# Kernel tuning notes

Hardware: AMD Instinct MI355X
Metric: run time of the kernel (lower is better)

Reference implementation:

```python
import jax, jax.numpy as jnp
import numpy as np

OUTPUT_LEN = 128

def setup_inputs() -> dict:
    key = jax.random.key(0)
    k1, k2, k3 = jax.random.split(key, 3)
    B, D = 256, 1024
    scale = 1.0 / np.sqrt(D)
    x = jax.random.normal(k1, (B, D), dtype=jnp.float32)
    W = jax.random.normal(k2, (D, 3 * D), dtype=jnp.float32) * scale  # input kernel [d, 3d] (z|r|h)
    U = jax.random.normal(k3, (D, 3 * D), dtype=jnp.float32) * scale  # recurrent kernel [d, 3d]
    b = jnp.zeros((3 * D,), dtype=jnp.float32)
    return {"x": x, "W": W, "U": U, "b": b}

def _gru_cell(inp, h, W, U, b):
    # Classic GRU (reset_after=False), Keras gate order z, r, h and
    # update rule h_new = z * h + (1 - z) * hh.
    gx = inp @ W + b              # [B, 3d]
    gh = h @ U                    # [B, 3d]
    xz, xr, xh = jnp.split(gx, 3, axis=-1)
    hz, hr, hh_lin = jnp.split(gh, 3, axis=-1)
    z = jax.nn.sigmoid(xz + hz)
    r = jax.nn.sigmoid(xr + hr)
    hh = jnp.tanh(xh + r * hh_lin)
    return z * h + (1.0 - z) * hh

def reference(x, W, U, b):
    # x: [B, d] is the initial GRU state; the first step's input is zeros,
    # afterwards each step's output (== new state) is fed back as input.
    def step(carry, _):
        inp, h = carry
        new_h = _gru_cell(inp, h, W, U, b)
        return (new_h, new_h), new_h

    init = (jnp.zeros_like(x), x)
    _, outs = jax.lax.scan(step, init, None, length=OUTPUT_LEN)  # [T, B, d]
    return jnp.transpose(outs, (1, 0, 2))  # [B, T, d]
```

## Files before the change

kernel.cpp:

```cpp
#include <hip/hip_runtime.h>
#include <stdint.h>

#define B_ROWS 256
#define DDIM   1024
#define TSTEPS 128
#define THREE_D 3072

typedef short bf16x8 __attribute__((ext_vector_type(8)));
typedef float f32x4  __attribute__((ext_vector_type(4)));
typedef unsigned short u16x8 __attribute__((ext_vector_type(8)));

static __device__ __forceinline__ unsigned short f2bf(float f) {
    union { float f; uint32_t u; } v; v.f = f;
    uint32_t u = v.u;
    uint32_t r = u + 0x7FFFu + ((u >> 16) & 1u);
    return (unsigned short)(r >> 16);
}
static __device__ __forceinline__ float bf2f(unsigned short h) {
    union { uint32_t u; float f; } v; v.u = ((uint32_t)h) << 16; return v.f;
}

__global__ __launch_bounds__(256) void pack_kernel(
    const float* __restrict__ W, const float* __restrict__ U,
    unsigned short* __restrict__ phi, unsigned short* __restrict__ plo)
{
    int t = blockIdx.x * 256 + threadIdx.x;
    int lane  = t & 63;
    int ktile = (t >> 6) & 31;
    int ntile = t >> 11;
    int col = ntile * 16 + (lane & 15);
    int q = col >> 10;
    int d = col & 1023;
    int k8 = ktile * 32 + ((lane >> 4) << 3);

    u16x8 ohi, olo;
    #pragma unroll
    for (int j = 0; j < 8; ++j) {
        int k = k8 + j;
        const float* wr = W + (size_t)k * THREE_D;
        const float* ur = U + (size_t)k * THREE_D;
        float v;
        if (q == 0)      v = wr[d] + ur[d];
        else if (q == 1) v = wr[1024 + d] + ur[1024 + d];
        else if (q == 2) v = wr[2048 + d];
        else             v = ur[2048 + d];
        unsigned short hi = f2bf(v);
        ohi[j] = hi;
        olo[j] = f2bf(v - bf2f(hi));
    }
    size_t base = ((size_t)(ntile * 32 + ktile) * 64 + lane) * 8;
    *(u16x8*)(phi + base) = ohi;
    *(u16x8*)(plo + base) = olo;
}

__global__ __launch_bounds__(256) void gru_step0(
    const float* __restrict__ x, const float* __restrict__ U,
    const float* __restrict__ bias,
    float* __restrict__ out,
    unsigned short* __restrict__ hbh, unsigned short* __restrict__ hbl)
{
    __shared__ float xt[16][64];
    const int tid = threadIdx.x;
    const int c   = tid & 63;
    const int rg  = tid >> 6;
    const int dt  = blockIdx.x & 15;
    const int rt  = blockIdx.x >> 4;

    float acc[4][3];
    #pragma unroll
    for (int rr = 0; rr < 4; ++rr) { acc[rr][0] = 0.f; acc[rr][1] = 0.f; acc[rr][2] = 0.f; }

    for (int kc = 0; kc < 16; ++kc) {
        #pragma unroll
        for (int i = 0; i < 4; ++i) {
            int e = i * 256 + tid;
            int row = e >> 6, kk = e & 63;
            xt[row][kk] = x[(size_t)(rt * 16 + row) * DDIM + kc * 64 + kk];
        }
        __syncthreads();
        #pragma unroll 4
        for (int kk = 0; kk < 64; ++kk) {
            int k = kc * 64 + kk;
            const float* up = U + (size_t)k * THREE_D + dt * 64 + c;
            float uz = up[0], ur = up[1024], uh = up[2048];
            #pragma unroll
            for (int rr = 0; rr < 4; ++rr) {
                float xv = xt[rg * 4 + rr][kk];
                acc[rr][0] += xv * uz;
                acc[rr][1] += xv * ur;
                acc[rr][2] += xv * uh;
            }
        }
        __syncthreads();
    }

    int d = dt * 64 + c;
    #pragma unroll
    for (int rr = 0; rr < 4; ++rr) {
        int row = rt * 16 + rg * 4 + rr;
        float z  = 1.0f / (1.0f + __expf(-(acc[rr][0] + bias[d])));
        float r  = 1.0f / (1.0f + __expf(-(acc[rr][1] + bias[1024 + d])));
        float hh = tanhf(bias[2048 + d] + r * acc[rr][2]);
        float hp = x[(size_t)row * DDIM + d];
        float hn = z * hp + (1.0f - z) * hh;
        out[(size_t)row * (TSTEPS * DDIM) + d] = hn;
        unsigned short hi = f2bf(hn);
        size_t off = (size_t)row * DDIM + d;
        hbh[off] = hi;
        hbl[off] = f2bf(hn - bf2f(hi));
    }
}

__global__ __launch_bounds__(256) void gru_step(
    const unsigned short* __restrict__ phi,
    const unsigned short* __restrict__ plo,
    const unsigned short* __restrict__ hbh_in,
    const unsigned short* __restrict__ hbl_in,
    const float* __restrict__ bias,
    float* __restrict__ out,
    unsigned short* __restrict__ hbh_out,
    unsigned short* __restrict__ hbl_out,
    int t)
{
    __shared__ float gbuf[4][64][16];
    const int tid  = threadIdx.x;
    const int lane = tid & 63;
    const int q    = tid >> 6;
    const int dt   = blockIdx.x & 63;
    const int rt   = blockIdx.x >> 6;
    const int llow = lane & 15;
    const int lhi  = lane >> 4;

    f32x4 acc[4] = {f32x4{0,0,0,0}, f32x4{0,0,0,0}, f32x4{0,0,0,0}, f32x4{0,0,0,0}};

    const int ntile = q * 64 + dt;
    const unsigned short* bhp = phi + ((size_t)ntile * 2048 + lane) * 8;
    const unsigned short* blp = plo + ((size_t)ntile * 2048 + lane) * 8;
    const unsigned short* ahp = hbh_in + (size_t)(rt * 64 + llow) * DDIM + lhi * 8;
    const unsigned short* alp = hbl_in + (size_t)(rt * 64 + llow) * DDIM + lhi * 8;

    #pragma unroll 2
    for (int kt = 0; kt < 32; ++kt) {
        bf16x8 bh = *(const bf16x8*)(bhp + (size_t)kt * 512);
        bf16x8 bl = *(const bf16x8*)(blp + (size_t)kt * 512);
        const int koff = kt * 32;
        #pragma unroll
        for (int m = 0; m < 4; ++m) {
            bf16x8 ah = *(const bf16x8*)(ahp + (size_t)m * 16 * DDIM + koff);
            bf16x8 al = *(const bf16x8*)(alp + (size_t)m * 16 * DDIM + koff);
            acc[m] = __builtin_amdgcn_mfma_f32_16x16x32_bf16(ah, bh, acc[m], 0, 0, 0);
            acc[m] = __builtin_amdgcn_mfma_f32_16x16x32_bf16(al, bh, acc[m], 0, 0, 0);
            acc[m] = __builtin_amdgcn_mfma_f32_16x16x32_bf16(ah, bl, acc[m], 0, 0, 0);
        }
    }

    #pragma unroll
    for (int m = 0; m < 4; ++m) {
        #pragma unroll
        for (int r = 0; r < 4; ++r) {
            gbuf[q][m * 16 + lhi * 4 + r][llow] = acc[m][r];
        }
    }
    __syncthreads();

    #pragma unroll
    for (int i = 0; i < 4; ++i) {
        int e = tid + i * 256;
        int row = e >> 4, col = e & 15;
        int d = dt * 16 + col;
        int grow = rt * 64 + row;
        float gz = gbuf[0][row][col] + bias[d];
        float gr = gbuf[1][row][col] + bias[1024 + d];
        float gx = gbuf[2][row][col] + bias[2048 + d];
        float gu = gbuf[3][row][col];
        float z  = 1.0f / (1.0f + __expf(-gz));
        float r  = 1.0f / (1.0f + __expf(-gr));
        float hh = tanhf(gx + r * gu);
        size_t orow = (size_t)grow * (TSTEPS * DDIM);
        float hp = out[orow + (size_t)(t - 1) * DDIM + d];
        float hn = z * hp + (1.0f - z) * hh;
        out[orow + (size_t)t * DDIM + d] = hn;
        unsigned short hi = f2bf(hn);
        size_t hoff = (size_t)grow * DDIM + d;
        hbh_out[hoff] = hi;
        hbl_out[hoff] = f2bf(hn - bf2f(hi));
    }
}

extern "C" void kernel_launch(void* const* d_in, const int* in_sizes, int n_in,
                              void* d_out, int out_size, void* d_ws, size_t ws_size,
                              hipStream_t stream) {
    const float* x = (const float*)d_in[0];
    const float* W = (const float*)d_in[1];
    const float* U = (const float*)d_in[2];
    const float* b = (const float*)d_in[3];
    float* out = (float*)d_out;

    char* ws = (char*)d_ws;
    unsigned short* phi = (unsigned short*)ws;
    unsigned short* plo = (unsigned short*)(ws + (8u << 20));
    char* hbase = ws + (16u << 20);
    unsigned short* hbh[2] = { (unsigned short*)hbase,
                               (unsigned short*)(hbase + (512u << 10)) };
    unsigned short* hbl[2] = { (unsigned short*)(hbase + (1024u << 10)),
                               (unsigned short*)(hbase + (1536u << 10)) };

    hipLaunchKernelGGL(pack_kernel, dim3(2048), dim3(256), 0, stream, W, U, phi, plo);
    hipLaunchKernelGGL(gru_step0, dim3(256), dim3(256), 0, stream, x, U, b,
                       out, hbh[0], hbl[0]);

    for (int t = 1; t < TSTEPS; ++t) {
        int src = (t - 1) & 1;
        int dst = t & 1;
        hipLaunchKernelGGL(gru_step, dim3(256), dim3(256), 0, stream,
                           phi, plo, hbh[src], hbl[src], b,
                           out, hbh[dst], hbl[dst], t);
    }
}
```

Measured before the change: 4.673 ms.

## Fuse all GRU steps into one persistent cooperative kernel with resident weights

Replaces the pack kernel, step-0 kernel and 127 per-step launches with a single cooperative persistent kernel of 256 blocks. Each block keeps its slice of the packed weights on chip for all steps, the high bf16 half in LDS and the low half in registers, and keeps the previous state in registers. Steps are separated by per-row-group atomic counter barriers instead of kernel boundaries. This removes launch overhead and the repeated weight reads from global memory, at the cost of spin-wait barriers, high register and LDS pressure, and a reliance on all 256 blocks being co-resident.

```diff
diff --git a/kernel.cpp b/kernel.cpp
--- a/kernel.cpp
+++ b/kernel.cpp
@@ -1,14 +1,13 @@
 #include <hip/hip_runtime.h>
 #include <stdint.h>
 
-#define B_ROWS 256
-#define DDIM   1024
-#define TSTEPS 128
+
+#define DDIM    1024
 #define THREE_D 3072
+#define TSTEPS  128
 
 typedef short bf16x8 __attribute__((ext_vector_type(8)));
 typedef float f32x4  __attribute__((ext_vector_type(4)));
-typedef unsigned short u16x8 __attribute__((ext_vector_type(8)));
 
 static __device__ __forceinline__ unsigned short f2bf(float f) {
     union { float f; uint32_t u; } v; v.f = f;
@@ -19,110 +18,25 @@
 static __device__ __forceinline__ float bf2f(unsigned short h) {
     union { uint32_t u; float f; } v; v.u = ((uint32_t)h) << 16; return v.f;
 }
-
-__global__ __launch_bounds__(256) void pack_kernel(
-    const float* __restrict__ W, const float* __restrict__ U,
-    unsigned short* __restrict__ phi, unsigned short* __restrict__ plo)
-{
-    int t = blockIdx.x * 256 + threadIdx.x;
-    int lane  = t & 63;
-    int ktile = (t >> 6) & 31;
-    int ntile = t >> 11;
-    int col = ntile * 16 + (lane & 15);
-    int q = col >> 10;
-    int d = col & 1023;
-    int k8 = ktile * 32 + ((lane >> 4) << 3);
-
-    u16x8 ohi, olo;
+static __device__ __forceinline__ void split8(const float* v, bf16x8& hi, bf16x8& lo) {
     #pragma unroll
     for (int j = 0; j < 8; ++j) {
-        int k = k8 + j;
-        const float* wr = W + (size_t)k * THREE_D;
-        const float* ur = U + (size_t)k * THREE_D;
-        float v;
-        if (q == 0)      v = wr[d] + ur[d];
-        else if (q == 1) v = wr[1024 + d] + ur[1024 + d];
-        else if (q == 2) v = wr[2048 + d];
-        else             v = ur[2048 + d];
-        unsigned short hi = f2bf(v);
-        ohi[j] = hi;
-        olo[j] = f2bf(v - bf2f(hi));
-    }
-    size_t base = ((size_t)(ntile * 32 + ktile) * 64 + lane) * 8;
-    *(u16x8*)(phi + base) = ohi;
-    *(u16x8*)(plo + base) = olo;
-}
-
-__global__ __launch_bounds__(256) void gru_step0(
-    const float* __restrict__ x, const float* __restrict__ U,
-    const float* __restrict__ bias,
-    float* __restrict__ out,
-    unsigned short* __restrict__ hbh, unsigned short* __restrict__ hbl)
+        unsigned short h = f2bf(v[j]);
+        hi[j] = (short)h;
+        lo[j] = (short)f2bf(v[j] - bf2f(h));
+    }
+}
+
+__global__ __launch_bounds__(256, 1) void gru_persistent(
+    const float* __restrict__ x, const float* __restrict__ W,
+    const float* __restrict__ U, const float* __restrict__ bias,
+    float* __restrict__ out, unsigned short* __restrict__ hb,
+    int* __restrict__ syncc)
 {
-    __shared__ float xt[16][64];
-    const int tid = threadIdx.x;
-    const int c   = tid & 63;
-    const int rg  = tid >> 6;
-    const int dt  = blockIdx.x & 15;
-    const int rt  = blockIdx.x >> 4;
-
-    float acc[4][3];
-    #pragma unroll
-    for (int rr = 0; rr < 4; ++rr) { acc[rr][0] = 0.f; acc[rr][1] = 0.f; acc[rr][2] = 0.f; }
-
-    for (int kc = 0; kc < 16; ++kc) {
-        #pragma unroll
-        for (int i = 0; i < 4; ++i) {
-            int e = i * 256 + tid;
-            int row = e >> 6, kk = e & 63;
-            xt[row][kk] = x[(size_t)(rt * 16 + row) * DDIM + kc * 64 + kk];
-        }
-        __syncthreads();
-        #pragma unroll 4
-        for (int kk = 0; kk < 64; ++kk) {
-            int k = kc * 64 + kk;
-            const float* up = U + (size_t)k * THREE_D + dt * 64 + c;
-            float uz = up[0], ur = up[1024], uh = up[2048];
-            #pragma unroll
-            for (int rr = 0; rr < 4; ++rr) {
-                float xv = xt[rg * 4 + rr][kk];
-                acc[rr][0] += xv * uz;
-                acc[rr][1] += xv * ur;
-                acc[rr][2] += xv * uh;
-            }
-        }
-        __syncthreads();
-    }
-
-    int d = dt * 64 + c;
-    #pragma unroll
-    for (int rr = 0; rr < 4; ++rr) {
-        int row = rt * 16 + rg * 4 + rr;
-        float z  = 1.0f / (1.0f + __expf(-(acc[rr][0] + bias[d])));
-        float r  = 1.0f / (1.0f + __expf(-(acc[rr][1] + bias[1024 + d])));
-        float hh = tanhf(bias[2048 + d] + r * acc[rr][2]);
-        float hp = x[(size_t)row * DDIM + d];
-        float hn = z * hp + (1.0f - z) * hh;
-        out[(size_t)row * (TSTEPS * DDIM) + d] = hn;
-        unsigned short hi = f2bf(hn);
-        size_t off = (size_t)row * DDIM + d;
-        hbh[off] = hi;
-        hbl[off] = f2bf(hn - bf2f(hi));
-    }
-}
-
-__global__ __launch_bounds__(256) void gru_step(
-    const unsigned short* __restrict__ phi,
-    const unsigned short* __restrict__ plo,
-    const unsigned short* __restrict__ hbh_in,
-    const unsigned short* __restrict__ hbl_in,
-    const float* __restrict__ bias,
-    float* __restrict__ out,
-    unsigned short* __restrict__ hbh_out,
-    unsigned short* __restrict__ hbl_out,
-    int t)
-{
-    __shared__ float gbuf[4][64][16];
+    extern __shared__ char smem[];
+    unsigned short* whi = (unsigned short*)smem;
+    float* gbuf = (float*)(smem + 131072);
+
     const int tid  = threadIdx.x;
     const int lane = tid & 63;
     const int q    = tid >> 6;
@@ -130,60 +44,148 @@
     const int rt   = blockIdx.x >> 6;
     const int llow = lane & 15;
     const int lhi  = lane >> 4;
-
-    f32x4 acc[4] = {f32x4{0,0,0,0}, f32x4{0,0,0,0}, f32x4{0,0,0,0}, f32x4{0,0,0,0}};
-
-    const int ntile = q * 64 + dt;
-    const unsigned short* bhp = phi + ((size_t)ntile * 2048 + lane) * 8;
-    const unsigned short* blp = plo + ((size_t)ntile * 2048 + lane) * 8;
-    const unsigned short* ahp = hbh_in + (size_t)(rt * 64 + llow) * DDIM + lhi * 8;
-    const unsigned short* alp = hbl_in + (size_t)(rt * 64 + llow) * DDIM + lhi * 8;
-
-    #pragma unroll 2
-    for (int kt = 0; kt < 32; ++kt) {
-        bf16x8 bh = *(const bf16x8*)(bhp + (size_t)kt * 512);
-        bf16x8 bl = *(const bf16x8*)(blp + (size_t)kt * 512);
-        const int koff = kt * 32;
-        #pragma unroll
-        for (int m = 0; m < 4; ++m) {
-            bf16x8 ah = *(const bf16x8*)(ahp + (size_t)m * 16 * DDIM + koff);
-            bf16x8 al = *(const bf16x8*)(alp + (size_t)m * 16 * DDIM + koff);
-            acc[m] = __builtin_amdgcn_mfma_f32_16x16x32_bf16(ah, bh, acc[m], 0, 0, 0);
-            acc[m] = __builtin_amdgcn_mfma_f32_16x16x32_bf16(al, bh, acc[m], 0, 0, 0);
-            acc[m] = __builtin_amdgcn_mfma_f32_16x16x32_bf16(ah, bl, acc[m], 0, 0, 0);
-        }
-    }
-
-    #pragma unroll
-    for (int m = 0; m < 4; ++m) {
-        #pragma unroll
-        for (int r = 0; r < 4; ++r) {
-            gbuf[q][m * 16 + lhi * 4 + r][llow] = acc[m][r];
-        }
-    }
-    __syncthreads();
-
+    const int d    = dt * 16 + llow;
+
+    bf16x8 wlo[32];
+    {
+        const int cc = (q == 0) ? d : (q == 1) ? (1024 + d) : (2048 + d);
+        const float* m1 = (q == 3) ? U : W;
+        #pragma unroll
+        for (int kt = 0; kt < 32; ++kt) {
+            float v[8];
+            #pragma unroll
+            for (int j = 0; j < 8; ++j) {
+                int k = kt * 32 + lhi * 8 + j;
+                float val = m1[(size_t)k * THREE_D + cc];
+                if (q <= 1) val += U[(size_t)k * THREE_D + cc];
+                v[j] = val;
+            }
+            bf16x8 bh, bl;
+            split8(v, bh, bl);
+            *(bf16x8*)(whi + ((q * 32 + kt) * 64 + lane) * 8) = bh;
+            wlo[kt] = bl;
+        }
+    }
+
+    const int erow = tid >> 4;
+    const int ecol = tid & 15;
+    const int dd   = dt * 16 + ecol;
+    const float bz = bias[dd];
+    const float br = bias[1024 + dd];
+    const float bx = bias[2048 + dd];
+    size_t ooff[4], hoff[4];
+    float hprev[4];
     #pragma unroll
     for (int i = 0; i < 4; ++i) {
-        int e = tid + i * 256;
-        int row = e >> 4, col = e & 15;
-        int d = dt * 16 + col;
-        int grow = rt * 64 + row;
-        float gz = gbuf[0][row][col] + bias[d];
-        float gr = gbuf[1][row][col] + bias[1024 + d];
-        float gx = gbuf[2][row][col] + bias[2048 + d];
-        float gu = gbuf[3][row][col];
-        float z  = 1.0f / (1.0f + __expf(-gz));
-        float r  = 1.0f / (1.0f + __expf(-gr));
-        float hh = tanhf(gx + r * gu);
-        size_t orow = (size_t)grow * (TSTEPS * DDIM);
-        float hp = out[orow + (size_t)(t - 1) * DDIM + d];
-        float hn = z * hp + (1.0f - z) * hh;
-        out[orow + (size_t)t * DDIM + d] = hn;
-        unsigned short hi = f2bf(hn);
-        size_t hoff = (size_t)grow * DDIM + d;
-        hbh_out[hoff] = hi;
-        hbl_out[hoff] = f2bf(hn - bf2f(hi));
+        int grow = rt * 64 + erow + i * 16;
+        ooff[i]  = (size_t)grow * (TSTEPS * DDIM) + dd;
+        hoff[i]  = (size_t)grow * DDIM + dd;
+        hprev[i] = x[(size_t)grow * DDIM + dd];
+    }
+    __syncthreads();
+
+    auto epilogue = [&](int t, f32x4* acc, unsigned short* dh, unsigned short* dl) {
+        #pragma unroll
+        for (int m = 0; m < 4; ++m)
+            #pragma unroll
+            for (int r = 0; r < 4; ++r)
+                gbuf[(q * 64 + m * 16 + lhi * 4 + r) * 17 + llow] = acc[m][r];
+        __syncthreads();
+        #pragma unroll
+        for (int i = 0; i < 4; ++i) {
+            int row = erow + i * 16;
+            float gz = gbuf[(0 * 64 + row) * 17 + ecol] + bz;
+            float gr = gbuf[(1 * 64 + row) * 17 + ecol] + br;
+            float gx = gbuf[(2 * 64 + row) * 17 + ecol] + bx;
+            float gu = gbuf[(3 * 64 + row) * 17 + ecol];
+            float z  = 1.0f / (1.0f + __expf(-gz));
+            float r_ = 1.0f / (1.0f + __expf(-gr));
+            float hh = tanhf(gx + r_ * gu);
+            float hn = z * hprev[i] + (1.0f - z) * hh;
+            hprev[i] = hn;
+            out[ooff[i] + (size_t)t * DDIM] = hn;
+            unsigned short hi = f2bf(hn);
+            dh[hoff[i]] = hi;
+            dl[hoff[i]] = f2bf(hn - bf2f(hi));
+        }
+    };
+
+    auto barrier = [&](int t) {
+        __threadfence();
+        __syncthreads();
+        if (tid == 0) {
+            int* c = syncc + (t * 4 + rt) * 16;
+            __hip_atomic_fetch_add(c, 1, __ATOMIC_RELEASE, __HIP_MEMORY_SCOPE_AGENT);
+            while (__hip_atomic_load(c, __ATOMIC_RELAXED, __HIP_MEMORY_SCOPE_AGENT) < 64)
+                __builtin_amdgcn_s_sleep(2);
+            __threadfence();
+        }
+        __syncthreads();
+    };
+
+    const unsigned short* wbase = whi + ((q * 32) * 64 + lane) * 8;
+
+    {
+        f32x4 acc[4] = {f32x4{0,0,0,0}, f32x4{0,0,0,0}, f32x4{0,0,0,0}, f32x4{0,0,0,0}};
+        if (q != 2) {
+            const float* xb = x + (size_t)(rt * 64 + llow) * DDIM + lhi * 8;
+            const float* ub = U + ((q == 0) ? d : (q == 1) ? (1024 + d) : (2048 + d));
+            #pragma unroll
+            for (int kt = 0; kt < 32; ++kt) {
+                bf16x8 bh, bl;
+                if (q == 3) {
+                    bh = *(const bf16x8*)(wbase + kt * 512);
+                    bl = wlo[kt];
+                } else {
+                    float v[8];
+                    #pragma unroll
+                    for (int j = 0; j < 8; ++j)
+                        v[j] = ub[(size_t)(kt * 32 + lhi * 8 + j) * THREE_D];
+                    split8(v, bh, bl);
+                }
+                #pragma unroll
+                for (int m = 0; m < 4; ++m) {
+                    float a[8];
+                    const float* ap = xb + (size_t)m * 16 * DDIM + kt * 32;
+                    #pragma unroll
+                    for (int j = 0; j < 8; ++j) a[j] = ap[j];
+                    bf16x8 ah, al;
+                    split8(a, ah, al);
+                    acc[m] = __builtin_amdgcn_mfma_f32_16x16x32_bf16(ah, bh, acc[m], 0, 0, 0);
+                    acc[m] = __builtin_amdgcn_mfma_f32_16x16x32_bf16(al, bh, acc[m], 0, 0, 0);
+                    acc[m] = __builtin_amdgcn_mfma_f32_16x16x32_bf16(ah, bl, acc[m], 0, 0, 0);
+                }
+            }
+        }
+        epilogue(0, acc, hb, hb + 262144);
+        barrier(0);
+    }
+
+    for (int t = 1; t < TSTEPS; ++t) {
+        const unsigned short* sh = hb + (size_t)((t - 1) & 1) * 524288;
+        const unsigned short* sl = sh + 262144;
+        unsigned short* dh = hb + (size_t)(t & 1) * 524288;
+        unsigned short* dl = dh + 262144;
+        const unsigned short* ahp = sh + (size_t)(rt * 64 + llow) * DDIM + lhi * 8;
+        const unsigned short* alp = sl + (size_t)(rt * 64 + llow) * DDIM + lhi * 8;
+
+        f32x4 acc[4] = {f32x4{0,0,0,0}, f32x4{0,0,0,0}, f32x4{0,0,0,0}, f32x4{0,0,0,0}};
+        #pragma unroll
+        for (int kt = 0; kt < 32; ++kt) {
+            bf16x8 bh = *(const bf16x8*)(wbase + kt * 512);
+            bf16x8 bl = wlo[kt];
+            const int koff = kt * 32;
+            #pragma unroll
+            for (int m = 0; m < 4; ++m) {
+                bf16x8 ah = *(const bf16x8*)(ahp + (size_t)m * 16 * DDIM + koff);
+                bf16x8 al = *(const bf16x8*)(alp + (size_t)m * 16 * DDIM + koff);
+                acc[m] = __builtin_amdgcn_mfma_f32_16x16x32_bf16(ah, bh, acc[m], 0, 0, 0);
+                acc[m] = __builtin_amdgcn_mfma_f32_16x16x32_bf16(al, bh, acc[m], 0, 0, 0);
+                acc[m] = __builtin_amdgcn_mfma_f32_16x16x32_bf16(ah, bl, acc[m], 0, 0, 0);
+            }
+        }
+        epilogue(t, acc, dh, dl);
+        if (t < TSTEPS - 1) barrier(t);
     }
 }
 
@@ -196,24 +198,13 @@
     const float* b = (const float*)d_in[3];
     float* out = (float*)d_out;
 
-    char* ws = (char*)d_ws;
-    unsigned short* phi = (unsigned short*)ws;
-    unsigned short* plo = (unsigned short*)(ws + (8u << 20));
-    char* hbase = ws + (16u << 20);
-    unsigned short* hbh[2] = { (unsigned short*)hbase,
-                               (unsigned short*)(hbase + (512u << 10)) };
-    unsigned short* hbl[2] = { (unsigned short*)(hbase + (1024u << 10)),
-                               (unsigned short*)(hbase + (1536u << 10)) };
-
-    hipLaunchKernelGGL(pack_kernel, dim3(2048), dim3(256), 0, stream, W, U, phi, plo);
-    hipLaunchKernelGGL(gru_step0, dim3(256), dim3(256), 0, stream, x, U, b,
-                       out, hbh[0], hbl[0]);
-
-    for (int t = 1; t < TSTEPS; ++t) {
-        int src = (t - 1) & 1;
-        int dst = t & 1;
-        hipLaunchKernelGGL(gru_step, dim3(256), dim3(256), 0, stream,
-                           phi, plo, hbh[src], hbl[src], b,
-                           out, hbh[dst], hbl[dst], t);
-    }
-}
+    unsigned short* hb = (unsigned short*)d_ws;
+    int* syncc = (int*)((char*)d_ws + (2u << 20));
+
+    hipMemsetAsync(syncc, 0, 8192 * sizeof(int), stream);
+
+    void* kargs[] = { (void*)&x, (void*)&W, (void*)&U, (void*)&b,
+                      (void*)&out, (void*)&hb, (void*)&syncc };
+    hipLaunchCooperativeKernel((const void*)gru_persistent, dim3(256), dim3(256),
+                               kargs, 148480, stream);
+}
```

Measured after the change: 9.372 ms. +100.5%, slower.
